# Optimization experiments

Hardware: AMD Instinct MI355X
Metric: run time of the kernel (lower is better)

## Reference

```python
import jax, jax.numpy as jnp
import numpy as np

N = 50000      # nodes
E = 800000     # edges (avg degree 16)
D_IN = 32      # raw feature dim
D = 96         # hidden == out dim (residual requires equality)
L = 4          # number of GatedGCN layers
NC = 10        # n_classes
EPS = 1e-6


def _w(k, shape, fan_in):
    return jax.random.normal(k, shape, jnp.float32) / np.sqrt(fan_in).astype(np.float32)


def setup_inputs() -> dict:
    key = jax.random.key(0)
    ks = jax.random.split(key, 16)
    inp = {
        'h': jax.random.normal(ks[0], (N, D_IN), jnp.float32),
        'e': jax.random.normal(ks[1], (E, D_IN), jnp.float32),
        'src': jax.random.randint(ks[2], (E,), 0, N, jnp.int32),
        'dst': jax.random.randint(ks[3], (E,), 0, N, jnp.int32),
        'fp_w': _w(ks[4], (D_IN, D), D_IN), 'fp_b': jnp.zeros((D,), jnp.float32),
        'ep_w': _w(ks[5], (D_IN, D), D_IN), 'ep_b': jnp.zeros((D,), jnp.float32),
    }
    for i, name in enumerate(['A', 'B', 'C', 'D', 'E']):
        inp[name + '_w'] = _w(ks[6 + i], (L, D, D), D)
        inp[name + '_b'] = jnp.zeros((L, D), jnp.float32)
    inp['mlp0_w'] = _w(ks[11], (D, D // 2), D); inp['mlp0_b'] = jnp.zeros((D // 2,), jnp.float32)
    inp['mlp1_w'] = _w(ks[12], (D // 2, D // 4), D // 2); inp['mlp1_b'] = jnp.zeros((D // 4,), jnp.float32)
    inp['mlp2_w'] = _w(ks[13], (D // 4, NC), D // 4); inp['mlp2_b'] = jnp.zeros((NC,), jnp.float32)
    return inp


def reference(h, e, src, dst, fp_w, fp_b, ep_w, ep_b,
              A_w, A_b, B_w, B_b, C_w, C_b, D_w, D_b, E_w, E_b,
              mlp0_w, mlp0_b, mlp1_w, mlp1_b, mlp2_w, mlp2_b):
    # input projections
    h = h @ fp_w + fp_b                       # [N, D]
    e = e @ ep_w + ep_b                       # [E, D]

    def layer(carry, p):
        h, e = carry
        Aw, Ab, Bw, Bb, Cw, Cb, Dw, Db, Ew, Eb = p
        Ah = h @ Aw + Ab
        Bh = h @ Bw + Bb
        Ce = e @ Cw + Cb
        Dh = h @ Dw + Db
        Eh = h @ Ew + Eb
        # edge gate: e_ij = D h_i + E h_j + C e_ij  (u_add_v with u=src, v=dst)
        e_new = Dh[src] + Eh[dst] + Ce          # [E, D]
        sigma = jax.nn.sigmoid(e_new)           # [E, D]
        # gated aggregation to destination nodes
        num = jax.ops.segment_sum(Bh[src] * sigma, dst, num_segments=N)  # [N, D]
        den = jax.ops.segment_sum(sigma, dst, num_segments=N)            # [N, D]
        h_new = Ah + num / (den + EPS)
        # relu then residual (batch_norm=False, dropout eval no-op)
        return (h + jax.nn.relu(h_new), e + jax.nn.relu(e_new)), None

    (h, e), _ = jax.lax.scan(layer, (h, e),
                             (A_w, A_b, B_w, B_b, C_w, C_b, D_w, D_b, E_w, E_b))

    # MLPReadout (L=2 halvings) + sigmoid head
    y = jax.nn.relu(h @ mlp0_w + mlp0_b)
    y = jax.nn.relu(y @ mlp1_w + mlp1_b)
    y = y @ mlp2_w + mlp2_b
    return jax.nn.sigmoid(y)                    # [N, NC]
```

## Files before the change

kernel.cpp:

```cpp
#include <hip/hip_runtime.h>

#define NN 50000
#define NE 800000
#define DIN 32
#define DD 96
#define NL 4
#define NCLS 10
#define EPSF 1e-6f

typedef unsigned short u16;
typedef unsigned int u32;

typedef __bf16 bf16x8 __attribute__((ext_vector_type(8)));
typedef float f32x4 __attribute__((ext_vector_type(4)));

static __device__ __forceinline__ u16 f2bf(float f) {
    u32 x = __float_as_uint(f);
    x += 0x7FFFu + ((x >> 16) & 1u);
    return (u16)(x >> 16);
}
static __device__ __forceinline__ u32 pk2(float a, float b) {
    u32 r;
    asm("v_cvt_pk_bf16_f32 %0, %1, %2" : "=v"(r) : "v"(a), "v"(b));
    return r;
}
static __device__ __forceinline__ float unlo(u32 u) { return __uint_as_float(u << 16); }
static __device__ __forceinline__ float unhi(u32 u) { return __uint_as_float(u & 0xFFFF0000u); }
static __device__ __forceinline__ float frcp(float x) { return __builtin_amdgcn_rcpf(x); }

__global__ void k_zero4(int* __restrict__ p, long n4) {
    long i = (long)blockIdx.x * blockDim.x + threadIdx.x;
    if (i < n4) ((int4*)p)[i] = make_int4(0, 0, 0, 0);
}

__global__ void k_hist(const int* __restrict__ dst, int* __restrict__ counts) {
    int i = blockIdx.x * blockDim.x + threadIdx.x;
    if (i < NE) atomicAdd(&counts[dst[i]], 1);
}

__global__ __launch_bounds__(1024) void k_scan1(const int* __restrict__ counts,
                                                int* __restrict__ excl,
                                                int* __restrict__ bsum, int n) {
    __shared__ int wsum[16];
    const int tid = threadIdx.x, lane = tid & 63, wid = tid >> 6;
    const int i = blockIdx.x * 1024 + tid;
    int v = (i < n) ? counts[i] : 0;
    int x = v;
#pragma unroll
    for (int off = 1; off < 64; off <<= 1) {
        int t = __shfl_up(x, (unsigned)off, 64);
        if (lane >= off) x += t;
    }
    if (lane == 63) wsum[wid] = x;
    __syncthreads();
    if (tid < 16) {
        int s = wsum[tid];
#pragma unroll
        for (int off = 1; off < 16; off <<= 1) {
            int t = __shfl_up(s, (unsigned)off, 16);
            if (tid >= off) s += t;
        }
        wsum[tid] = s;
    }
    __syncthreads();
    const int wbase = wid ? wsum[wid - 1] : 0;
    if (i < n) excl[i] = wbase + x - v;
    if (tid == 1023) bsum[blockIdx.x] = wbase + x;
}

__global__ void k_scan2(int* __restrict__ bsum, int nb) {
    const int lane = threadIdx.x;
    int v = (lane < nb) ? bsum[lane] : 0;
    int x = v;
#pragma unroll
    for (int off = 1; off < 64; off <<= 1) {
        int t = __shfl_up(x, (unsigned)off, 64);
        if (lane >= off) x += t;
    }
    if (lane < nb) bsum[lane] = x - v;
}

__global__ void k_scan3(int* __restrict__ row_ptr, int* __restrict__ cursor,
                        const int* __restrict__ bsum, int n) {
    int i = blockIdx.x * blockDim.x + threadIdx.x;
    if (i < n) {
        int v = row_ptr[i] + bsum[i >> 10];
        row_ptr[i] = v;
        cursor[i] = v;
    }
    if (i == 0) row_ptr[n] = NE;
}

__global__ void k_scatter(const int* __restrict__ src, const int* __restrict__ dst,
                          int* __restrict__ cursor, int* __restrict__ eperm,
                          int* __restrict__ srcp) {
    int i = blockIdx.x * blockDim.x + threadIdx.x;
    if (i >= NE) return;
    int pos = atomicAdd(&cursor[dst[i]], 1);
    eperm[pos] = i;
    srcp[pos] = src[i];
}

__global__ void k_packAll(const float* __restrict__ A_w, const float* __restrict__ B_w,
                          const float* __restrict__ C_w, const float* __restrict__ D_w,
                          const float* __restrict__ E_w,
                          const float* __restrict__ fp_w, const float* __restrict__ ep_w,
                          const float* __restrict__ m0w,
                          u16* __restrict__ awf, u16* __restrict__ bwf, u16* __restrict__ cwf,
                          u16* __restrict__ dwf, u16* __restrict__ ewf,
                          u16* __restrict__ wfp, u16* __restrict__ wep,
                          float* __restrict__ w0p) {
    const int PER = NL * 6 * 3 * 64;
    int q = blockIdx.x * blockDim.x + threadIdx.x;
    if (q < 5 * PER) {
        int which = q / PER;
        int qq = q - which * PER;
        const float* W_all = which == 0 ? A_w : which == 1 ? B_w : which == 2 ? C_w
                           : which == 3 ? D_w : E_w;
        u16* wf = which == 0 ? awf : which == 1 ? bwf : which == 2 ? cwf
                : which == 3 ? dwf : ewf;
        int l = qq / (6 * 3 * 64);
        int rem = qq - l * (6 * 3 * 64);
        int tile = rem / (3 * 64);
        int rem2 = rem - tile * (3 * 64);
        int c = rem2 >> 6, ln = rem2 & 63;
        const float* W = W_all + (long)l * DD * DD;
        int n = tile * 16 + (ln & 15);
        int k0 = c * 32 + (ln >> 4) * 8;
        u16 wv[8];
#pragma unroll
        for (int j = 0; j < 8; ++j) {
            int kk = k0 + j;
            int kact = (kk % 6) * 16 + kk / 6;
            wv[j] = f2bf(W[kact * DD + n]);
        }
        *(uint4*)&wf[(long)qq * 8] = *(uint4*)wv;
    } else if (q < 5 * PER + 768) {
        int qq = q - 5 * PER;
        int which = qq / 384; qq -= which * 384;
        const float* W = which ? ep_w : fp_w;
        u16* wf = which ? wep : wfp;
        int ln = qq & 63;
        int n = (qq >> 6) * 16 + (ln & 15);
        int k0 = (ln >> 4) * 8;
        u16 wv[8];
#pragma unroll
        for (int j = 0; j < 8; ++j) wv[j] = f2bf(W[(k0 + j) * DD + n]);
        *(uint4*)&wf[qq * 8] = *(uint4*)wv;
    } else {
        int qq = q - 5 * PER - 768;
        if (qq < DD * 48) {
            int p = qq / 48, j = qq - p * 48;
            int jp = (p % 6) * 16 + p / 6;
            w0p[qq] = m0w[jp * 48 + j];
        }
    }
}

template <bool BFOUT, bool PERM, bool POUT>
__global__ __launch_bounds__(256) void k_proj_m(const float* __restrict__ X,
                                                const u16* __restrict__ wf,
                                                const float* __restrict__ B,
                                                void* __restrict__ Y,
                                                const int* __restrict__ eperm,
                                                int ntiles) {
    const int lane = threadIdx.x & 63;
    const int gw = (blockIdx.x * blockDim.x + threadIdx.x) >> 6;
    const int nw = (gridDim.x * blockDim.x) >> 6;
    const int lm = lane & 15, quad = lane >> 4;

    bf16x8 bfr[6];
    float bias[6];
#pragma unroll
    for (int t = 0; t < 6; ++t) {
        bfr[t] = *(const bf16x8*)&wf[(t * 64 + lane) * 8];
        bias[t] = B[t * 16 + lm];
    }

    for (int tile = gw; tile < ntiles; tile += nw) {
        const int row = tile * 16 + lm;
        const long srow = PERM ? (long)eperm[row] : (long)row;
        float4 x0 = *(const float4*)&X[srow * DIN + quad * 8];
        float4 x1 = *(const float4*)&X[srow * DIN + quad * 8 + 4];
        u32 ap[4] = {pk2(x0.x, x0.y), pk2(x0.z, x0.w), pk2(x1.x, x1.y), pk2(x1.z, x1.w)};
        bf16x8 af = *(bf16x8*)ap;
        f32x4 acc[6];
#pragma unroll
        for (int t = 0; t < 6; ++t) {
            acc[t] = (f32x4){bias[t], bias[t], bias[t], bias[t]};
            acc[t] = __builtin_amdgcn_mfma_f32_16x16x32_bf16(af, bfr[t], acc[t], 0, 0, 0);
        }
        const long rbase = (long)tile * 16 + quad * 4;
        if (POUT) {
#pragma unroll
            for (int r = 0; r < 4; ++r) {
                if (BFOUT) {
                    u16* p = (u16*)Y + (rbase + r) * DD + lm * 6;
                    *(u32*)p       = pk2(acc[0][r], acc[1][r]);
                    *(u32*)(p + 2) = pk2(acc[2][r], acc[3][r]);
                    *(u32*)(p + 4) = pk2(acc[4][r], acc[5][r]);
                } else {
                    float* p = (float*)Y + (rbase + r) * DD + lm * 6;
                    *(float2*)(p)     = make_float2(acc[0][r], acc[1][r]);
                    *(float2*)(p + 2) = make_float2(acc[2][r], acc[3][r]);
                    *(float2*)(p + 4) = make_float2(acc[4][r], acc[5][r]);
                }
            }
        } else {
#pragma unroll
            for (int t = 0; t < 6; ++t) {
                const int j = t * 16 + lm;
#pragma unroll
                for (int r = 0; r < 4; ++r) {
                    float v = acc[t][r];
                    if (BFOUT) ((u16*)Y)[(rbase + r) * DD + j] = f2bf(v);
                    else       ((float*)Y)[(rbase + r) * DD + j] = v;
                }
            }
        }
    }
}

__global__ __launch_bounds__(256) void k_gemm4m(const float* __restrict__ X,
                                                const u16* __restrict__ awf, const float* __restrict__ ab,
                                                const u16* __restrict__ bwf, const float* __restrict__ bb,
                                                const u16* __restrict__ dwf, const float* __restrict__ db,
                                                const u16* __restrict__ ewf, const float* __restrict__ eb,
                                                float* __restrict__ Y0, u16* __restrict__ Y1,
                                                u16* __restrict__ Y2, u16* __restrict__ Y3,
                                                int ntiles) {
    const int lane = threadIdx.x & 63;
    const int w = threadIdx.x >> 6;
    const int lm = lane & 15, quad = lane >> 4;
    const u16* wf = (w == 0) ? awf : (w == 1) ? bwf : (w == 2) ? dwf : ewf;
    const float* bp = (w == 0) ? ab : (w == 1) ? bb : (w == 2) ? db : eb;

    bf16x8 bfr[6][3];
    float bias[6];
#pragma unroll
    for (int t = 0; t < 6; ++t) {
#pragma unroll
        for (int c = 0; c < 3; ++c)
            bfr[t][c] = *(const bf16x8*)&wf[((t * 3 + c) * 64 + lane) * 8];
        bias[t] = bp[t * 16 + lm];
    }

    for (int tile = blockIdx.x; tile < ntiles; tile += gridDim.x) {
        const float* xr = X + (long)(tile * 16 + lm) * DD;
        bf16x8 a[3];
#pragma unroll
        for (int c = 0; c < 3; ++c) {
            float4 x0 = *(const float4*)&xr[c * 32 + quad * 8];
            float4 x1 = *(const float4*)&xr[c * 32 + quad * 8 + 4];
            u32 ap[4] = {pk2(x0.x, x0.y), pk2(x0.z, x0.w), pk2(x1.x, x1.y), pk2(x1.z, x1.w)};
            a[c] = *(bf16x8*)ap;
        }
        f32x4 acc[6];
#pragma unroll
        for (int t = 0; t < 6; ++t) {
            acc[t] = (f32x4){bias[t], bias[t], bias[t], bias[t]};
#pragma unroll
            for (int c = 0; c < 3; ++c)
                acc[t] = __builtin_amdgcn_mfma_f32_16x16x32_bf16(a[c], bfr[t][c], acc[t], 0, 0, 0);
        }
        const long rbase = (long)tile * 16 + quad * 4;
        if (w == 0) {
#pragma unroll
            for (int r = 0; r < 4; ++r) {
                float* p = Y0 + (rbase + r) * DD + lm * 6;
                *(float2*)(p)     = make_float2(acc[0][r], acc[1][r]);
                *(float2*)(p + 2) = make_float2(acc[2][r], acc[3][r]);
                *(float2*)(p + 4) = make_float2(acc[4][r], acc[5][r]);
            }
        } else {
            u16* Yp = (w == 1) ? Y1 : (w == 2) ? Y2 : Y3;
#pragma unroll
            for (int r = 0; r < 4; ++r) {
                u16* p = Yp + (rbase + r) * DD + lm * 6;
                *(u32*)p       = pk2(acc[0][r], acc[1][r]);
                *(u32*)(p + 2) = pk2(acc[2][r], acc[3][r]);
                *(u32*)(p + 4) = pk2(acc[4][r], acc[5][r]);
            }
        }
    }
}

__global__ __launch_bounds__(256) void k_node_edge_w(u16* ebuf,
                                                     const u16* __restrict__ cwf,
                                                     const float* __restrict__ Cb,
                                                     const u16* __restrict__ Dh,
                                                     const u16* __restrict__ Eh,
                                                     const u16* __restrict__ Bh,
                                                     const int* __restrict__ srcp,
                                                     const int* __restrict__ row_ptr,
                                                     const float* __restrict__ Ah,
                                                     float* __restrict__ hbuf) {
    const int lane = threadIdx.x & 63;
    const int gw = (blockIdx.x * blockDim.x + threadIdx.x) >> 6;
    const int nw = (gridDim.x * blockDim.x) >> 6;
    const int lm = lane & 15, quad = lane >> 4;

    bf16x8 bfrag[6][3];
    float cb[6];
#pragma unroll
    for (int t = 0; t < 6; ++t) {
#pragma unroll
        for (int c = 0; c < 3; ++c)
            bfrag[t][c] = *(const bf16x8*)&cwf[((t * 3 + c) * 64 + lane) * 8];
        cb[t] = Cb[t * 16 + lm];
    }

    for (int n = gw; n < NN; n += nw) {
        const int r0 = row_ptr[n], r1 = row_ptr[n + 1];
        if (r0 >= r1) continue;
        float eh[6];
        {
            const u16* ep = Eh + (long)n * DD + lm * 6;
            u32 e0 = *(const u32*)ep, e1 = *(const u32*)(ep + 2), e2 = *(const u32*)(ep + 4);
            eh[0] = unlo(e0); eh[1] = unhi(e0); eh[2] = unlo(e1);
            eh[3] = unhi(e1); eh[4] = unlo(e2); eh[5] = unhi(e2);
        }
        float nacc[6] = {0.f, 0.f, 0.f, 0.f, 0.f, 0.f};
        float dacc[6] = {0.f, 0.f, 0.f, 0.f, 0.f, 0.f};

        bf16x8 a[3];
        {
            const int rows = r1 - r0 < 16 ? r1 - r0 : 16;
            const long arow = r0 + (lm < rows ? lm : 0);
#pragma unroll
            for (int c = 0; c < 3; ++c)
                a[c] = *(const bf16x8*)&ebuf[arow * DD + c * 32 + quad * 8];
        }

        for (int chunk = r0; chunk < r1; chunk += 16) {
            const int rows = r1 - chunk < 16 ? r1 - chunk : 16;
            int sr[4];
#pragma unroll
            for (int r = 0; r < 4; ++r) {
                int rl = quad * 4 + r;
                sr[r] = (chunk + rl < r1) ? srcp[chunk + rl] : 0;
            }
            f32x4 acc[6];
#pragma unroll
            for (int t = 0; t < 6; ++t) {
                acc[t] = (f32x4){cb[t], cb[t], cb[t], cb[t]};
#pragma unroll
                for (int c = 0; c < 3; ++c)
                    acc[t] = __builtin_amdgcn_mfma_f32_16x16x32_bf16(a[c], bfrag[t][c], acc[t], 0, 0, 0);
            }
            const int nchunk = chunk + 16;
            if (nchunk < r1) {
                const int rows2 = r1 - nchunk < 16 ? r1 - nchunk : 16;
                const long arow2 = nchunk + (lm < rows2 ? lm : 0);
#pragma unroll
                for (int c = 0; c < 3; ++c)
                    a[c] = *(const bf16x8*)&ebuf[arow2 * DD + c * 32 + quad * 8];
            }
#pragma unroll
            for (int r = 0; r < 4; ++r) {
                const int rl = quad * 4 + r;
                if (rl < rows) {
                    const long s = sr[r];
                    const u16* dp = Dh + s * DD + lm * 6;
                    const u16* bp = Bh + s * DD + lm * 6;
                    u16* ep = ebuf + (long)(chunk + rl) * DD + lm * 6;
                    u32 d0 = *(const u32*)dp, d1 = *(const u32*)(dp + 2), d2 = *(const u32*)(dp + 4);
                    u32 b0 = *(const u32*)bp, b1 = *(const u32*)(bp + 2), b2 = *(const u32*)(bp + 4);
                    u32 o0 = *(const u32*)ep, o1 = *(const u32*)(ep + 2), o2 = *(const u32*)(ep + 4);
                    float dh[6] = {unlo(d0), unhi(d0), unlo(d1), unhi(d1), unlo(d2), unhi(d2)};
                    float bh[6] = {unlo(b0), unhi(b0), unlo(b1), unhi(b1), unlo(b2), unhi(b2)};
                    float od[6] = {unlo(o0), unhi(o0), unlo(o1), unhi(o1), unlo(o2), unhi(o2)};
                    float ov[6];
#pragma unroll
                    for (int t = 0; t < 6; ++t) {
                        float en = acc[t][r] + dh[t] + eh[t];
                        float sg = frcp(1.f + __expf(-en));
                        nacc[t] += bh[t] * sg;
                        dacc[t] += sg;
                        ov[t] = od[t] + fmaxf(en, 0.f);
                    }
                    *(u32*)ep       = pk2(ov[0], ov[1]);
                    *(u32*)(ep + 2) = pk2(ov[2], ov[3]);
                    *(u32*)(ep + 4) = pk2(ov[4], ov[5]);
                }
            }
        }
#pragma unroll
        for (int t = 0; t < 6; ++t) {
            float x = nacc[t], y = dacc[t];
            x += __shfl_xor(x, 16); y += __shfl_xor(y, 16);
            x += __shfl_xor(x, 32); y += __shfl_xor(y, 32);
            nacc[t] = x; dacc[t] = y;
        }
        if (quad == 0) {
            const float* ap = Ah + (long)n * DD + lm * 6;
            float* hp = hbuf + (long)n * DD + lm * 6;
            float val[6];
#pragma unroll
            for (int t = 0; t < 6; ++t)
                val[t] = fmaxf(ap[t] + nacc[t] * frcp(dacc[t] + EPSF), 0.f);
            float2 h0 = *(float2*)hp, h1 = *(float2*)(hp + 2), h2 = *(float2*)(hp + 4);
            *(float2*)(hp)     = make_float2(h0.x + val[0], h0.y + val[1]);
            *(float2*)(hp + 2) = make_float2(h1.x + val[2], h1.y + val[3]);
            *(float2*)(hp + 4) = make_float2(h2.x + val[4], h2.y + val[5]);
        }
    }
}

__global__ void k_mlp(const float* __restrict__ X, const float* __restrict__ W,
                      const float* __restrict__ B, float* __restrict__ Y,
                      int K, int Dout, int act, long total) {
    long idx = (long)blockIdx.x * blockDim.x + threadIdx.x;
    if (idx >= total) return;
    int row = (int)(idx / Dout);
    int j = (int)(idx - (long)row * Dout);
    const float* xr = X + (long)row * K;
    float acc = B[j];
    for (int k = 0; k < K; ++k) acc = fmaf(xr[k], W[k * Dout + j], acc);
    if (act == 1) acc = fmaxf(acc, 0.f);
    else if (act == 2) acc = frcp(1.f + __expf(-acc));
    Y[idx] = acc;
}

extern "C" void kernel_launch(void* const* d_in, const int* in_sizes, int n_in,
                              void* d_out, int out_size, void* d_ws, size_t ws_size,
                              hipStream_t stream) {
    const float* h_in = (const float*)d_in[0];
    const float* e_in = (const float*)d_in[1];
    const int* src = (const int*)d_in[2];
    const int* dst = (const int*)d_in[3];
    const float* fp_w = (const float*)d_in[4];
    const float* fp_b = (const float*)d_in[5];
    const float* ep_w = (const float*)d_in[6];
    const float* ep_b = (const float*)d_in[7];
    const float* A_w = (const float*)d_in[8];
    const float* A_b = (const float*)d_in[9];
    const float* B_w = (const float*)d_in[10];
    const float* B_b = (const float*)d_in[11];
    const float* C_w = (const float*)d_in[12];
    const float* C_b = (const float*)d_in[13];
    const float* D_w = (const float*)d_in[14];
    const float* D_b = (const float*)d_in[15];
    const float* E_w = (const float*)d_in[16];
    const float* E_b = (const float*)d_in[17];
    const float* mlp0_w = (const float*)d_in[18];
    const float* mlp0_b = (const float*)d_in[19];
    const float* mlp1_w = (const float*)d_in[20];
    const float* mlp1_b = (const float*)d_in[21];
    const float* mlp2_w = (const float*)d_in[22];
    const float* mlp2_b = (const float*)d_in[23];
    float* out = (float*)d_out;

    const size_t ND_ = (size_t)NN * DD;
    const size_t ED_ = (size_t)NE * DD;
    const size_t FRAG = (size_t)NL * 6 * 3 * 64 * 8;
    char* w = (char*)d_ws;
    float* hbuf = (float*)w; w += ND_ * 4;
    float* Ahb  = (float*)w; w += ND_ * 4;
    u16* Bhb = (u16*)w; w += ND_ * 2;
    u16* Dhb = (u16*)w; w += ND_ * 2;
    u16* Ehb = (u16*)w; w += ND_ * 2;
    u16* ebuf = (u16*)w; w += ED_ * 2;
    int* counts  = (int*)w; w += (size_t)NN * 4;
    int* cursor  = (int*)w; w += (size_t)NN * 4;
    int* row_ptr = (int*)w; w += (size_t)(NN + 1) * 4 + 12;
    int* bsum    = (int*)w; w += 256;
    int* eperm   = (int*)w; w += (size_t)NE * 4;
    int* srcp    = (int*)w; w += (size_t)NE * 4;
    u16* awf = (u16*)w; w += FRAG * 2;
    u16* bwf = (u16*)w; w += FRAG * 2;
    u16* cwf = (u16*)w; w += FRAG * 2;
    u16* dwf = (u16*)w; w += FRAG * 2;
    u16* ewf = (u16*)w; w += FRAG * 2;
    u16* wfp = (u16*)w; w += (size_t)6 * 64 * 8 * 2;
    u16* wep = (u16*)w; w += (size_t)6 * 64 * 8 * 2;
    float* w0p = (float*)w; w += (size_t)DD * 48 * 4;
    size_t need = (size_t)(w - (char*)d_ws);
    if (ws_size < need) return;

    k_zero4<<<(NN / 4 + 255) / 256, 256, 0, stream>>>(counts, NN / 4);
    k_hist<<<(NE + 255) / 256, 256, 0, stream>>>(dst, counts);
    const int nsb = (NN + 1023) / 1024;
    k_scan1<<<nsb, 1024, 0, stream>>>(counts, row_ptr, bsum, NN);
    k_scan2<<<1, 64, 0, stream>>>(bsum, nsb);
    k_scan3<<<(NN + 255) / 256, 256, 0, stream>>>(row_ptr, cursor, bsum, NN);
    k_scatter<<<(NE + 255) / 256, 256, 0, stream>>>(src, dst, cursor, eperm, srcp);

    const int packTot = 5 * (NL * 6 * 3 * 64) + 768 + DD * 48;
    k_packAll<<<(packTot + 255) / 256, 256, 0, stream>>>(A_w, B_w, C_w, D_w, E_w,
                                                         fp_w, ep_w, mlp0_w,
                                                         awf, bwf, cwf, dwf, ewf,
                                                         wfp, wep, w0p);

    k_proj_m<false, false, true><<<256, 256, 0, stream>>>(h_in, wfp, fp_b, hbuf, nullptr, NN / 16);
    k_proj_m<true, true, true><<<2048, 256, 0, stream>>>(e_in, wep, ep_b, ebuf, eperm, NE / 16);

    const size_t LFRAG = (size_t)6 * 3 * 64 * 8;
    for (int l = 0; l < NL; ++l) {
        const float* Ab = A_b + (size_t)l * DD;
        const float* Bb = B_b + (size_t)l * DD;
        const float* Cb = C_b + (size_t)l * DD;
        const float* Db = D_b + (size_t)l * DD;
        const float* Eb = E_b + (size_t)l * DD;

        k_gemm4m<<<640, 256, 0, stream>>>(hbuf,
                                          awf + l * LFRAG, Ab, bwf + l * LFRAG, Bb,
                                          dwf + l * LFRAG, Db, ewf + l * LFRAG, Eb,
                                          Ahb, Bhb, Dhb, Ehb, NN / 16);
        k_node_edge_w<<<2560, 256, 0, stream>>>(ebuf, cwf + l * LFRAG, Cb, Dhb, Ehb, Bhb,
                                                srcp, row_ptr, Ahb, hbuf);
    }

    float* y1 = Ahb;
    float* y2 = Ahb + (size_t)NN * 48;
    long t0 = (long)NN * 48, t1 = (long)NN * 24, t2 = (long)NN * NCLS;
    k_mlp<<<(int)((t0 + 255) / 256), 256, 0, stream>>>(hbuf, w0p, mlp0_b, y1, DD, 48, 1, t0);
    k_mlp<<<(int)((t1 + 255) / 256), 256, 0, stream>>>(y1, mlp1_w, mlp1_b, y2, 48, 24, 1, t1);
    k_mlp<<<(int)((t2 + 255) / 256), 256, 0, stream>>>(y2, mlp2_w, mlp2_b, out, 24, NCLS, 2, t2);
}
```

Before: 1.285 ms.

## Move C-weight fragments to LDS, prefetch next node's edges, raise occupancy

The fused node/edge kernel now keeps the per-layer C weight fragments in shared memory instead of 18 bf16x8 registers per lane, and declares launch bounds with a minimum of 4 blocks to raise occupancy. It also prefetches the next node's row_ptr entries and first edge tile during the current node's last chunk, hiding load latency across node boundaries. The 4-way node GEMM launch grid is doubled. The trade is extra LDS reads per MFMA, and possible register spills under the tighter launch bound.

```diff
diff --git a/kernel.cpp b/kernel.cpp
--- a/kernel.cpp
+++ b/kernel.cpp
@@ -285,103 +285,122 @@
     }
 }
 
-__global__ __launch_bounds__(256) void k_node_edge_w(u16* ebuf,
-                                                     const u16* __restrict__ cwf,
-                                                     const float* __restrict__ Cb,
-                                                     const u16* __restrict__ Dh,
-                                                     const u16* __restrict__ Eh,
-                                                     const u16* __restrict__ Bh,
-                                                     const int* __restrict__ srcp,
-                                                     const int* __restrict__ row_ptr,
-                                                     const float* __restrict__ Ah,
-                                                     float* __restrict__ hbuf) {
+__global__ __launch_bounds__(256, 4) void k_node_edge_w(u16* ebuf,
+                                                        const u16* __restrict__ cwf,
+                                                        const float* __restrict__ Cb,
+                                                        const u16* __restrict__ Dh,
+                                                        const u16* __restrict__ Eh,
+                                                        const u16* __restrict__ Bh,
+                                                        const int* __restrict__ srcp,
+                                                        const int* __restrict__ row_ptr,
+                                                        const float* __restrict__ Ah,
+                                                        float* __restrict__ hbuf) {
+    __shared__ u16 cw_lds[6 * 3 * 64 * 8];
     const int lane = threadIdx.x & 63;
     const int gw = (blockIdx.x * blockDim.x + threadIdx.x) >> 6;
     const int nw = (gridDim.x * blockDim.x) >> 6;
     const int lm = lane & 15, quad = lane >> 4;
 
-    bf16x8 bfrag[6][3];
+    for (int idx = threadIdx.x; idx < 6 * 3 * 64; idx += 256)
+        ((uint4*)cw_lds)[idx] = ((const uint4*)cwf)[idx];
+    __syncthreads();
+
     float cb[6];
 #pragma unroll
-    for (int t = 0; t < 6; ++t) {
-#pragma unroll
-        for (int c = 0; c < 3; ++c)
-            bfrag[t][c] = *(const bf16x8*)&cwf[((t * 3 + c) * 64 + lane) * 8];
-        cb[t] = Cb[t * 16 + lm];
-    }
-
-    for (int n = gw; n < NN; n += nw) {
-        const int r0 = row_ptr[n], r1 = row_ptr[n + 1];
-        if (r0 >= r1) continue;
-        float eh[6];
-        {
-            const u16* ep = Eh + (long)n * DD + lm * 6;
-            u32 e0 = *(const u32*)ep, e1 = *(const u32*)(ep + 2), e2 = *(const u32*)(ep + 4);
-            eh[0] = unlo(e0); eh[1] = unhi(e0); eh[2] = unlo(e1);
-            eh[3] = unhi(e1); eh[4] = unlo(e2); eh[5] = unhi(e2);
-        }
+    for (int t = 0; t < 6; ++t) cb[t] = Cb[t * 16 + lm];
+
+    int n = gw;
+    int nr0 = 0, nr1 = 0;
+    if (n < NN) { nr0 = row_ptr[n]; nr1 = row_ptr[n + 1]; }
+    int pref_node = -1;
+    bf16x8 a[3];
+
+    while (n < NN) {
+        const int r0 = nr0, r1 = nr1;
+        const int n2 = n + nw;
+        if (n2 < NN) { nr0 = row_ptr[n2]; nr1 = row_ptr[n2 + 1]; }
+
         float nacc[6] = {0.f, 0.f, 0.f, 0.f, 0.f, 0.f};
         float dacc[6] = {0.f, 0.f, 0.f, 0.f, 0.f, 0.f};
 
-        bf16x8 a[3];
-        {
-            const int rows = r1 - r0 < 16 ? r1 - r0 : 16;
-            const long arow = r0 + (lm < rows ? lm : 0);
-#pragma unroll
-            for (int c = 0; c < 3; ++c)
-                a[c] = *(const bf16x8*)&ebuf[arow * DD + c * 32 + quad * 8];
-        }
-
-        for (int chunk = r0; chunk < r1; chunk += 16) {
-            const int rows = r1 - chunk < 16 ? r1 - chunk : 16;
-            int sr[4];
-#pragma unroll
-            for (int r = 0; r < 4; ++r) {
-                int rl = quad * 4 + r;
-                sr[r] = (chunk + rl < r1) ? srcp[chunk + rl] : 0;
-            }
-            f32x4 acc[6];
-#pragma unroll
-            for (int t = 0; t < 6; ++t) {
-                acc[t] = (f32x4){cb[t], cb[t], cb[t], cb[t]};
+        if (r0 < r1) {
+            float eh[6];
+            {
+                const u16* ep = Eh + (long)n * DD + lm * 6;
+                u32 e0 = *(const u32*)ep, e1 = *(const u32*)(ep + 2), e2 = *(const u32*)(ep + 4);
+                eh[0] = unlo(e0); eh[1] = unhi(e0); eh[2] = unlo(e1);
+                eh[3] = unhi(e1); eh[4] = unlo(e2); eh[5] = unhi(e2);
+            }
+            if (pref_node != n) {
+                const int rows = r1 - r0 < 16 ? r1 - r0 : 16;
+                const long arow = r0 + (lm < rows ? lm : 0);
 #pragma unroll
                 for (int c = 0; c < 3; ++c)
-                    acc[t] = __builtin_amdgcn_mfma_f32_16x16x32_bf16(a[c], bfrag[t][c], acc[t], 0, 0, 0);
-            }
-            const int nchunk = chunk + 16;
-            if (nchunk < r1) {
-                const int rows2 = r1 - nchunk < 16 ? r1 - nchunk : 16;
-                const long arow2 = nchunk + (lm < rows2 ? lm : 0);
-#pragma unroll
-                for (int c = 0; c < 3; ++c)
-                    a[c] = *(const bf16x8*)&ebuf[arow2 * DD + c * 32 + quad * 8];
-            }
-#pragma unroll
-            for (int r = 0; r < 4; ++r) {
-                const int rl = quad * 4 + r;
-                if (rl < rows) {
-                    const long s = sr[r];
-                    const u16* dp = Dh + s * DD + lm * 6;
-                    const u16* bp = Bh + s * DD + lm * 6;
-                    u16* ep = ebuf + (long)(chunk + rl) * DD + lm * 6;
-                    u32 d0 = *(const u32*)dp, d1 = *(const u32*)(dp + 2), d2 = *(const u32*)(dp + 4);
-                    u32 b0 = *(const u32*)bp, b1 = *(const u32*)(bp + 2), b2 = *(const u32*)(bp + 4);
-                    u32 o0 = *(const u32*)ep, o1 = *(const u32*)(ep + 2), o2 = *(const u32*)(ep + 4);
-                    float dh[6] = {unlo(d0), unhi(d0), unlo(d1), unhi(d1), unlo(d2), unhi(d2)};
-                    float bh[6] = {unlo(b0), unhi(b0), unlo(b1), unhi(b1), unlo(b2), unhi(b2)};
-                    float od[6] = {unlo(o0), unhi(o0), unlo(o1), unhi(o1), unlo(o2), unhi(o2)};
-                    float ov[6];
+                    a[c] = *(const bf16x8*)&ebuf[arow * DD + c * 32 + quad * 8];
+            }
+
+            for (int chunk = r0; chunk < r1; chunk += 16) {
+                const int rows = r1 - chunk < 16 ? r1 - chunk : 16;
+                int sr[4];
+#pragma unroll
+                for (int r = 0; r < 4; ++r) {
+                    int rl = quad * 4 + r;
+                    sr[r] = (chunk + rl < r1) ? srcp[chunk + rl] : 0;
+                }
+                f32x4 acc[6];
+#pragma unroll
+                for (int t = 0; t < 6; ++t)
+                    acc[t] = (f32x4){cb[t], cb[t], cb[t], cb[t]};
+#pragma unroll
+                for (int c = 0; c < 3; ++c) {
 #pragma unroll
                     for (int t = 0; t < 6; ++t) {
-                        float en = acc[t][r] + dh[t] + eh[t];
-                        float sg = frcp(1.f + __expf(-en));
-                        nacc[t] += bh[t] * sg;
-                        dacc[t] += sg;
-                        ov[t] = od[t] + fmaxf(en, 0.f);
+                        const bf16x8 bw = *(const bf16x8*)&cw_lds[((t * 3 + c) * 64 + lane) * 8];
+                        acc[t] = __builtin_amdgcn_mfma_f32_16x16x32_bf16(a[c], bw, acc[t], 0, 0, 0);
                     }
-                    *(u32*)ep       = pk2(ov[0], ov[1]);
-                    *(u32*)(ep + 2) = pk2(ov[2], ov[3]);
-                    *(u32*)(ep + 4) = pk2(ov[4], ov[5]);
+                }
+                const int nchunk = chunk + 16;
+                if (nchunk < r1) {
+                    const int rows2 = r1 - nchunk < 16 ? r1 - nchunk : 16;
+                    const long arow2 = nchunk + (lm < rows2 ? lm : 0);
+#pragma unroll
+                    for (int c = 0; c < 3; ++c)
+                        a[c] = *(const bf16x8*)&ebuf[arow2 * DD + c * 32 + quad * 8];
+                } else if (n2 < NN && nr0 < nr1) {
+                    const int rows2 = nr1 - nr0 < 16 ? nr1 - nr0 : 16;
+                    const long arow2 = nr0 + (lm < rows2 ? lm : 0);
+#pragma unroll
+                    for (int c = 0; c < 3; ++c)
+                        a[c] = *(const bf16x8*)&ebuf[arow2 * DD + c * 32 + quad * 8];
+                    pref_node = n2;
+                }
+#pragma unroll
+                for (int r = 0; r < 4; ++r) {
+                    const int rl = quad * 4 + r;
+                    if (rl < rows) {
+                        const long s = sr[r];
+                        const u16* dp = Dh + s * DD + lm * 6;
+                        const u16* bp = Bh + s * DD + lm * 6;
+                        u16* ep = ebuf + (long)(chunk + rl) * DD + lm * 6;
+                        u32 d0 = *(const u32*)dp, d1 = *(const u32*)(dp + 2), d2 = *(const u32*)(dp + 4);
+                        u32 b0 = *(const u32*)bp, b1 = *(const u32*)(bp + 2), b2 = *(const u32*)(bp + 4);
+                        u32 o0 = *(const u32*)ep, o1 = *(const u32*)(ep + 2), o2 = *(const u32*)(ep + 4);
+                        float dh[6] = {unlo(d0), unhi(d0), unlo(d1), unhi(d1), unlo(d2), unhi(d2)};
+                        float bh[6] = {unlo(b0), unhi(b0), unlo(b1), unhi(b1), unlo(b2), unhi(b2)};
+                        float od[6] = {unlo(o0), unhi(o0), unlo(o1), unhi(o1), unlo(o2), unhi(o2)};
+                        float ov[6];
+#pragma unroll
+                        for (int t = 0; t < 6; ++t) {
+                            float en = acc[t][r] + dh[t] + eh[t];
+                            float sg = frcp(1.f + __expf(-en));
+                            nacc[t] += bh[t] * sg;
+                            dacc[t] += sg;
+                            ov[t] = od[t] + fmaxf(en, 0.f);
+                        }
+                        *(u32*)ep       = pk2(ov[0], ov[1]);
+                        *(u32*)(ep + 2) = pk2(ov[2], ov[3]);
+                        *(u32*)(ep + 4) = pk2(ov[4], ov[5]);
+                    }
                 }
             }
         }
@@ -404,6 +423,7 @@
             *(float2*)(hp + 2) = make_float2(h1.x + val[2], h1.y + val[3]);
             *(float2*)(hp + 4) = make_float2(h2.x + val[4], h2.y + val[5]);
         }
+        n = n2;
     }
 }
 
@@ -503,10 +523,10 @@
         const float* Db = D_b + (size_t)l * DD;
         const float* Eb = E_b + (size_t)l * DD;
 
-        k_gemm4m<<<640, 256, 0, stream>>>(hbuf,
-                                          awf + l * LFRAG, Ab, bwf + l * LFRAG, Bb,
-                                          dwf + l * LFRAG, Db, ewf + l * LFRAG, Eb,
-                                          Ahb, Bhb, Dhb, Ehb, NN / 16);
+        k_gemm4m<<<1280, 256, 0, stream>>>(hbuf,
+                                           awf + l * LFRAG, Ab, bwf + l * LFRAG, Bb,
+                                           dwf + l * LFRAG, Db, ewf + l * LFRAG, Eb,
+                                           Ahb, Bhb, Dhb, Ehb, NN / 16);
         k_node_edge_w<<<2560, 256, 0, stream>>>(ebuf, cwf + l * LFRAG, Cb, Dhb, Ehb, Bhb,
                                                 srcp, row_ptr, Ahb, hbuf);
     }
```

After: 2.560 ms. 99.3% more time.
